# Kernel tuning notes

Measured on AMD Instinct MI355X. Metric: run time of the kernel, lower is better.

Reference implementation:

```python
import jax, jax.numpy as jnp
import numpy as np

B, N, D, G, K = 8, 4096, 64, 32, 16


def _knn_idx(pos, k, offset=1):
    # pos: (B, N, 3); exclude self via offset=1
    sq = jnp.sum(pos * pos, axis=-1)  # (B, N)
    dist = sq[:, :, None] + sq[:, None, :] - 2.0 * jnp.einsum('bnd,bmd->bnm', pos, pos)
    _, idx = jax.lax.top_k(-dist, k + offset)  # nearest first
    return idx[:, :, offset:]  # (B, N, k)


def _knn_group(x, idx):
    # x: (B, N, d), idx: (B, N, K) -> (B, N, K, d)
    return jax.vmap(lambda xb, ib: xb[ib])(x, idx)


def setup_inputs() -> dict:
    key = jax.random.key(0)
    ks = jax.random.split(key, 12)
    s = 0.02
    return {
        'x': jax.random.normal(ks[0], (B, N, D), jnp.float32),
        'pos': jax.random.normal(ks[1], (B, N, 3), jnp.float32),
        # layer_first: Linear(3d -> 4d) + relu, Linear(4d -> growth) + relu
        'W1': jax.random.normal(ks[2], (3 * D, 4 * D), jnp.float32) * s,
        'b1': jnp.zeros((4 * D,), jnp.float32),
        'W2': jax.random.normal(ks[3], (4 * D, G), jnp.float32) * s,
        'b2': jnp.zeros((G,), jnp.float32),
        # middle FCLayer: Linear(d+g -> g) + relu
        'Wmid': jax.random.normal(ks[4], (D + G, G), jnp.float32) * s,
        'bmid': jnp.zeros((G,), jnp.float32),
        # channel_gate2: Linear(d+2g -> d+2g)
        'Wg': jax.random.normal(ks[5], (D + 2 * G, D + 2 * G), jnp.float32) * s,
        'bg': jnp.zeros((D + 2 * G,), jnp.float32),
        # layer_last: Linear(d+2g -> g), no activation
        'Wlast': jax.random.normal(ks[6], (D + 2 * G, G), jnp.float32) * s,
        'blast': jnp.zeros((G,), jnp.float32),
    }


def reference(x, pos, W1, b1, W2, b2, Wmid, bmid, Wg, bg, Wlast, blast):
    knn_idx = _knn_idx(pos, K, offset=1)                 # (B, N, K)
    knn_feat = _knn_group(x, knn_idx)                    # (B, N, K, d)
    x_t = jnp.broadcast_to(x[:, :, None, :], knn_feat.shape)
    edge = jnp.concatenate([x_t, knn_feat, knn_feat - x_t], axis=-1)  # (B,N,K,3d)
    # layer_first: dense growth block
    h = jax.nn.relu(edge @ W1 + b1)
    h = jax.nn.relu(h @ W2 + b2)                          # (B,N,K,g)
    y = jnp.concatenate([h, x_t], axis=-1)               # (B,N,K,d+g)
    # middle layers (num_fc_layers-1 = 1 layer)
    y = jnp.concatenate([jax.nn.relu(y @ Wmid + bmid), y], axis=-1)  # (B,N,K,d+2g)
    # channel gate: mean over K, linear, sigmoid, scale
    gate = jax.nn.sigmoid(jnp.mean(y, axis=2) @ Wg + bg)  # (B,N,d+2g)
    y = y * gate[:, :, None, :]
    # layer_last (no activation) then concat
    y = jnp.concatenate([y @ Wlast + blast, y], axis=-1)   # (B,N,K,d+3g)
    # max aggregation over neighbors
    return jnp.max(y, axis=-2)                             # (B,N,d+3g)
```

## Files before the change

### kernel.cpp

```cpp
#include <hip/hip_runtime.h>
#include <stdint.h>

#define BB 8
#define NN 4096

typedef float f32x4 __attribute__((ext_vector_type(4)));
typedef short bf16x8 __attribute__((ext_vector_type(8)));
typedef bf16x8 bf16x8a __attribute__((may_alias));
#define MFMA16(a, b, c) __builtin_amdgcn_mfma_f32_16x16x32_bf16(a, b, c, 0, 0, 0)

static __device__ __forceinline__ short f2b(float f) {
    unsigned u = __float_as_uint(f);
    unsigned r = (u + 0x7FFFu + ((u >> 16) & 1u)) >> 16;
    return (short)r;
}
static __device__ __forceinline__ float b2f(short s) {
    return __uint_as_float(((unsigned)(unsigned short)s) << 16);
}
static __device__ __forceinline__ bf16x8 pack8(float4 a, float4 b) {
    bf16x8 v;
    v[0] = f2b(a.x); v[1] = f2b(a.y); v[2] = f2b(a.z); v[3] = f2b(a.w);
    v[4] = f2b(b.x); v[5] = f2b(b.y); v[6] = f2b(b.z); v[7] = f2b(b.w);
    return v;
}

__global__ __launch_bounds__(256)
void prep_kernel(const float* __restrict__ pos,
                 const float* __restrict__ W1, const float* __restrict__ W2,
                 const float* __restrict__ Wmid, const float* __restrict__ Wlast,
                 const float* __restrict__ Wg,
                 float4* __restrict__ pq,
                 short* __restrict__ W1T, short* __restrict__ W2T,
                 short* __restrict__ WmidT, short* __restrict__ WlastT,
                 short* __restrict__ WgT) {
    int t = blockIdx.x * 256 + threadIdx.x;
    if (t < 32768) {
        float x = pos[t * 3 + 0], y = pos[t * 3 + 1], z = pos[t * 3 + 2];
        float s = __fadd_rn(__fadd_rn(__fmul_rn(x, x), __fmul_rn(y, y)), __fmul_rn(z, z));
        pq[t] = make_float4(x, y, z, s);
    } else if (t < 81920) {
        int e = t - 32768; int col = e / 192, k = e - col * 192;
        W1T[e] = f2b(W1[(size_t)k * 256 + col]);
    } else if (t < 90112) {
        int e = t - 81920; int col = e >> 8, k = e & 255;
        W2T[e] = f2b(W2[(size_t)k * 32 + col]);
    } else if (t < 93184) {
        int e = t - 90112; int col = e / 96, k = e - col * 96;
        WmidT[e] = f2b(Wmid[(size_t)k * 32 + col]);
    } else if (t < 97280) {
        int e = t - 93184; int col = e >> 7, k = e & 127;
        WlastT[e] = f2b(Wlast[(size_t)k * 32 + col]);
    } else if (t < 113664) {
        int e = t - 97280; int col = e >> 7, k = e & 127;
        WgT[e] = f2b(Wg[(size_t)k * 128 + col]);
    }
}

static __device__ __forceinline__ float distf(float4 v, float qx, float qy,
                                              float qz, float qsq) {
    float dot = __fmaf_rn(v.z, qz, __fmaf_rn(v.y, qy, __fmul_rn(v.x, qx)));
    float d = __fsub_rn(__fadd_rn(qsq, v.w), __fmul_rn(2.0f, dot));
    return fmaxf(d, 0.0f);
}

__global__ __launch_bounds__(256)
void knn4_kernel(const float4* __restrict__ pq, int* __restrict__ out_idx) {
    __shared__ unsigned long long comp[4][160];

    const int w = threadIdx.x >> 6;
    const int l = threadIdx.x & 63;
    const int q = blockIdx.x * 4 + w;
    const int b = q >> 12, i = q & 4095;
    const int base = b << 12;
    const float INF = __uint_as_float(0x7F800000u);

    const float4 self = pq[base + i];
    const float qx = self.x, qy = self.y, qz = self.z, qsq = self.w;

    float lmin = INF;
#pragma unroll 4
    for (int t = 0; t < 64; ++t)
        lmin = fminf(lmin, distf(pq[base + t * 64 + l], qx, qy, qz, qsq));

    float cur = lmin, tau = INF;
    for (int r = 0; r < 17; ++r) {
        float m = cur;
#pragma unroll
        for (int o = 1; o < 64; o <<= 1) m = fminf(m, __shfl_xor(m, o));
        unsigned long long bal = __ballot(cur == m);
        if (l == (__ffsll((unsigned long long)bal) - 1)) cur = INF;
        tau = m;
    }

    int cbase = 0;
    const unsigned long long ltm = (l == 0) ? 0ull : ((~0ull) >> (64 - l));
    for (int t = 0; t < 64; ++t) {
        float d = distf(pq[base + t * 64 + l], qx, qy, qz, qsq);
        bool pr = (d <= tau);
        unsigned long long bb = __ballot(pr);
        if (pr) {
            int ps = cbase + __popcll(bb & ltm);
            if (ps < 160)
                comp[w][ps] = ((unsigned long long)__float_as_uint(d) << 32) |
                              (unsigned)(t * 64 + l);
        }
        cbase += __popcll(bb);
    }
    if (cbase > 160) cbase = 160;

    const unsigned long long INFK = ~0ull;
    unsigned long long ks[3];
#pragma unroll
    for (int s = 0; s < 3; ++s) {
        int e = s * 64 + l;
        ks[s] = (e < cbase) ? comp[w][e] : INFK;
    }
    unsigned keep = 0;
    for (int r = 0; r < 17; ++r) {
        unsigned long long ml = ks[0];
#pragma unroll
        for (int s = 1; s < 3; ++s) ml = (ks[s] < ml) ? ks[s] : ml;
        unsigned long long g = ml;
#pragma unroll
        for (int o = 1; o < 64; o <<= 1) {
            unsigned long long o2 = __shfl_xor(g, o);
            g = (o2 < g) ? o2 : g;
        }
        unsigned long long bb = __ballot(ml == g);
        if (l == (__ffsll(bb) - 1)) {
            bool done = false;
#pragma unroll
            for (int s = 0; s < 3; ++s)
                if (!done && ks[s] == g) { ks[s] = INFK; done = true; }
        }
        if (l == r - 1) keep = (unsigned)g;
    }
    if (l < 16) out_idx[(size_t)q * 16 + l] = (int)keep;
}

__global__ __launch_bounds__(256, 3)
void fused5_kernel(const float* __restrict__ x, const int* __restrict__ knn,
                   const short* __restrict__ W1T, const short* __restrict__ W2T,
                   const short* __restrict__ WmidT, const short* __restrict__ WlastT,
                   const short* __restrict__ WgT,
                   const float* __restrict__ b1, const float* __restrict__ b2,
                   const float* __restrict__ bmid, const float* __restrict__ bg,
                   const float* __restrict__ blast,
                   float* __restrict__ out) {
    __shared__ __align__(16) short s_h[64 * 264];
    __shared__ __align__(16) short s_y[64 * 136];
    __shared__ __align__(16) short s_ym[4 * 128];
    __shared__ float s_gate[4][128];

    const int w = threadIdx.x >> 6;
    const int l = threadIdx.x & 63;
    const int c16 = l & 15;
    const int qa = l >> 4;
    const int p = blockIdx.x * 4 + w;
    const int b = p >> 12;

    {
        const float* xrow = x + (size_t)p * 64;
        float4 xa = *(const float4*)(xrow + qa * 8);
        float4 xb = *(const float4*)(xrow + qa * 8 + 4);
        float4 xc = *(const float4*)(xrow + 32 + qa * 8);
        float4 xd = *(const float4*)(xrow + 32 + qa * 8 + 4);
        int nb = knn[(size_t)p * 16 + c16] & 4095;
        const float* nrow = x + ((size_t)(b << 12) + nb) * 64;
        float4 na = *(const float4*)(nrow + qa * 8);
        float4 nb4 = *(const float4*)(nrow + qa * 8 + 4);
        float4 nc = *(const float4*)(nrow + 32 + qa * 8);
        float4 nd = *(const float4*)(nrow + 32 + qa * 8 + 4);
        float4 da, db, dc, dd;
        da.x = na.x - xa.x; da.y = na.y - xa.y; da.z = na.z - xa.z; da.w = na.w - xa.w;
        db.x = nb4.x - xb.x; db.y = nb4.y - xb.y; db.z = nb4.z - xb.z; db.w = nb4.w - xb.w;
        dc.x = nc.x - xc.x; dc.y = nc.y - xc.y; dc.z = nc.z - xc.z; dc.w = nc.w - xc.w;
        dd.x = nd.x - xd.x; dd.y = nd.y - xd.y; dd.z = nd.z - xd.z; dd.w = nd.w - xd.w;
        bf16x8 pxa = pack8(xa, xb), pxc = pack8(xc, xd);
        int row = w * 16 + c16;
        short* sr = s_h + row * 264;
        *(bf16x8a*)(sr + qa * 8)       = pxa;
        *(bf16x8a*)(sr + 32 + qa * 8)  = pxc;
        *(bf16x8a*)(sr + 64 + qa * 8)  = pack8(na, nb4);
        *(bf16x8a*)(sr + 96 + qa * 8)  = pack8(nc, nd);
        *(bf16x8a*)(sr + 128 + qa * 8) = pack8(da, db);
        *(bf16x8a*)(sr + 160 + qa * 8) = pack8(dc, dd);
        short* yr = s_y + row * 136;
        *(bf16x8a*)(yr + 64 + qa * 8)  = pxa;
        *(bf16x8a*)(yr + 96 + qa * 8)  = pxc;
    }
    __syncthreads();

    f32x4 acc[4][4];
#pragma unroll
    for (int n = 0; n < 4; ++n) {
        float bv = b1[w * 64 + n * 16 + c16];
#pragma unroll
        for (int m = 0; m < 4; ++m) acc[m][n] = (f32x4){bv, bv, bv, bv};
    }
    {
        const short* w1p = W1T + (size_t)(w * 64 + c16) * 192 + qa * 8;
#pragma unroll
        for (int t = 0; t < 6; ++t) {
            bf16x8 av[4], bw[4];
#pragma unroll
            for (int m = 0; m < 4; ++m)
                av[m] = *(const bf16x8a*)(s_h + (m * 16 + c16) * 264 + t * 32 + qa * 8);
#pragma unroll
            for (int n = 0; n < 4; ++n)
                bw[n] = *(const bf16x8a*)(w1p + (size_t)n * 3072 + t * 32);
#pragma unroll
            for (int m = 0; m < 4; ++m)
#pragma unroll
                for (int n = 0; n < 4; ++n)
                    acc[m][n] = MFMA16(av[m], bw[n], acc[m][n]);
        }
    }
    __syncthreads();

#pragma unroll
    for (int m = 0; m < 4; ++m)
#pragma unroll
        for (int n = 0; n < 4; ++n)
#pragma unroll
            for (int r = 0; r < 4; ++r)
                s_h[(m * 16 + qa * 4 + r) * 264 + w * 64 + n * 16 + c16] =
                    f2b(fmaxf(acc[m][n][r], 0.f));
    __syncthreads();

    {
        f32x4 hacc[2];
        float h0 = b2[c16], h1v = b2[16 + c16];
        hacc[0] = (f32x4){h0, h0, h0, h0};
        hacc[1] = (f32x4){h1v, h1v, h1v, h1v};
#pragma unroll
        for (int t = 0; t < 8; ++t) {
            bf16x8 am = *(const bf16x8a*)(s_h + (w * 16 + c16) * 264 + t * 32 + qa * 8);
            bf16x8 wb0 = *(const bf16x8a*)(W2T + (size_t)c16 * 256 + t * 32 + qa * 8);
            bf16x8 wb1 = *(const bf16x8a*)(W2T + (size_t)(16 + c16) * 256 + t * 32 + qa * 8);
            hacc[0] = MFMA16(am, wb0, hacc[0]);
            hacc[1] = MFMA16(am, wb1, hacc[1]);
        }
#pragma unroll
        for (int n2 = 0; n2 < 2; ++n2)
#pragma unroll
            for (int r = 0; r < 4; ++r)
                s_y[(w * 16 + qa * 4 + r) * 136 + 32 + n2 * 16 + c16] =
                    f2b(fmaxf(hacc[n2][r], 0.f));
    }

    {
        f32x4 macc[2];
        float m0 = bmid[c16], m1 = bmid[16 + c16];
        macc[0] = (f32x4){m0, m0, m0, m0};
        macc[1] = (f32x4){m1, m1, m1, m1};
#pragma unroll
        for (int t = 0; t < 3; ++t) {
            bf16x8 av = *(const bf16x8a*)(s_y + (w * 16 + c16) * 136 + 32 + t * 32 + qa * 8);
            bf16x8 wb0 = *(const bf16x8a*)(WmidT + (size_t)c16 * 96 + t * 32 + qa * 8);
            bf16x8 wb1 = *(const bf16x8a*)(WmidT + (size_t)(16 + c16) * 96 + t * 32 + qa * 8);
            macc[0] = MFMA16(av, wb0, macc[0]);
            macc[1] = MFMA16(av, wb1, macc[1]);
        }
#pragma unroll
        for (int n2 = 0; n2 < 2; ++n2)
#pragma unroll
            for (int r = 0; r < 4; ++r)
                s_y[(w * 16 + qa * 4 + r) * 136 + n2 * 16 + c16] =
                    f2b(fmaxf(macc[n2][r], 0.f));
    }
    __syncthreads();

    {
        float s0 = 0.f, s1 = 0.f;
#pragma unroll
        for (int k = 0; k < 16; ++k) {
            const short* yp = s_y + (w * 16 + k) * 136;
            s0 += b2f(yp[2 * l]);
            s1 += b2f(yp[2 * l + 1]);
        }
        s_ym[w * 128 + 2 * l]     = f2b(s0 * 0.0625f);
        s_ym[w * 128 + 2 * l + 1] = f2b(s1 * 0.0625f);
    }
    __syncthreads();

    {
        f32x4 gacc[2];
        float g0 = bg[w * 32 + c16], g1 = bg[w * 32 + 16 + c16];
        gacc[0] = (f32x4){g0, g0, g0, g0};
        gacc[1] = (f32x4){g1, g1, g1, g1};
#pragma unroll
        for (int t = 0; t < 4; ++t) {
            bf16x8 av = *(const bf16x8a*)(s_ym + (c16 & 3) * 128 + t * 32 + qa * 8);
            bf16x8 wb0 = *(const bf16x8a*)(WgT + (size_t)(w * 32 + c16) * 128 + t * 32 + qa * 8);
            bf16x8 wb1 = *(const bf16x8a*)(WgT + (size_t)(w * 32 + 16 + c16) * 128 + t * 32 + qa * 8);
            gacc[0] = MFMA16(av, wb0, gacc[0]);
            gacc[1] = MFMA16(av, wb1, gacc[1]);
        }
        if (qa == 0) {
#pragma unroll
            for (int n2 = 0; n2 < 2; ++n2)
#pragma unroll
                for (int r = 0; r < 4; ++r)
                    s_gate[r][w * 32 + n2 * 16 + c16] =
                        1.0f / (1.0f + __expf(-gacc[n2][r]));
        }
    }
    __syncthreads();

    {
        float g0 = s_gate[w][2 * l], g1 = s_gate[w][2 * l + 1];
        float m0 = -__uint_as_float(0x7F800000u), m1 = m0;
#pragma unroll
        for (int k = 0; k < 16; ++k) {
            short* yp = s_y + (w * 16 + k) * 136;
            float v0 = b2f(yp[2 * l]) * g0;
            float v1 = b2f(yp[2 * l + 1]) * g1;
            m0 = fmaxf(m0, v0);
            m1 = fmaxf(m1, v1);
            yp[2 * l]     = f2b(v0);
            yp[2 * l + 1] = f2b(v1);
        }
        float2 st; st.x = m0; st.y = m1;
        *(float2*)(out + (size_t)p * 160 + 32 + 2 * l) = st;
    }
    __syncthreads();

    {
        f32x4 zacc[2];
        float z0 = blast[c16], z1 = blast[16 + c16];
        zacc[0] = (f32x4){z0, z0, z0, z0};
        zacc[1] = (f32x4){z1, z1, z1, z1};
#pragma unroll
        for (int t = 0; t < 4; ++t) {
            bf16x8 av = *(const bf16x8a*)(s_y + (w * 16 + c16) * 136 + t * 32 + qa * 8);
            bf16x8 wb0 = *(const bf16x8a*)(WlastT + (size_t)c16 * 128 + t * 32 + qa * 8);
            bf16x8 wb1 = *(const bf16x8a*)(WlastT + (size_t)(16 + c16) * 128 + t * 32 + qa * 8);
            zacc[0] = MFMA16(av, wb0, zacc[0]);
            zacc[1] = MFMA16(av, wb1, zacc[1]);
        }
#pragma unroll
        for (int nt = 0; nt < 2; ++nt) {
            float m = fmaxf(fmaxf(zacc[nt][0], zacc[nt][1]),
                            fmaxf(zacc[nt][2], zacc[nt][3]));
            m = fmaxf(m, __shfl_xor(m, 16));
            m = fmaxf(m, __shfl_xor(m, 32));
            if (l < 16) out[(size_t)p * 160 + nt * 16 + l] = m;
        }
    }
}

extern "C" void kernel_launch(void* const* d_in, const int* in_sizes, int n_in,
                              void* d_out, int out_size, void* d_ws, size_t ws_size,
                              hipStream_t stream) {
    const float* x     = (const float*)d_in[0];
    const float* pos   = (const float*)d_in[1];
    const float* W1    = (const float*)d_in[2];
    const float* b1    = (const float*)d_in[3];
    const float* W2    = (const float*)d_in[4];
    const float* b2    = (const float*)d_in[5];
    const float* Wmid  = (const float*)d_in[6];
    const float* bmid  = (const float*)d_in[7];
    const float* Wg    = (const float*)d_in[8];
    const float* bg    = (const float*)d_in[9];
    const float* Wlast = (const float*)d_in[10];
    const float* blast = (const float*)d_in[11];
    float* out = (float*)d_out;

    char* ws = (char*)d_ws;
    int*    idx    = (int*)(ws + 0);
    float4* pq     = (float4*)(ws + 2097152);
    short*  W1T    = (short*)(ws + 2621440);
    short*  W2T    = (short*)(ws + 2719744);
    short*  WmidT  = (short*)(ws + 2736128);
    short*  WlastT = (short*)(ws + 2742272);
    short*  WgT    = (short*)(ws + 2750464);

    prep_kernel<<<dim3(444), dim3(256), 0, stream>>>(
        pos, W1, W2, Wmid, Wlast, Wg, pq, W1T, W2T, WmidT, WlastT, WgT);
    knn4_kernel<<<dim3(BB * NN / 4), dim3(256), 0, stream>>>(pq, idx);
    fused5_kernel<<<dim3(BB * NN / 4), dim3(256), 0, stream>>>(
        x, idx, W1T, W2T, WmidT, WlastT, WgT, b1, b2, bmid, bg, blast, out);
}
```

Measured before the change: 507.4 us.

## Fuse KNN into MLP kernel, fold W1 edge weights, dedupe per-point x features

Moves the KNN search into the fused MLP kernel, so neighbor indices pass through a wave shuffle rather than a global buffer and a separate launch. Folds the [x, n, n-x] @ W1 concat algebraically into a 128-wide weight VT = [W1a-W1c; W1b+W1c], cutting the first GEMM's K dimension from 192 to 128. Also stores the per-point x (constant across the 16 neighbors) once per wave instead of per row, shrinking s_y and the gating/mean work. Risks higher register and LDS pressure in the combined kernel, plus small bf16 rounding differences from the pre-summed weights.

```diff
diff --git a/kernel.cpp b/kernel.cpp
--- a/kernel.cpp
+++ b/kernel.cpp
@@ -30,7 +30,7 @@
                  const float* __restrict__ Wmid, const float* __restrict__ Wlast,
                  const float* __restrict__ Wg,
                  float4* __restrict__ pq,
-                 short* __restrict__ W1T, short* __restrict__ W2T,
+                 short* __restrict__ VT, short* __restrict__ W2T,
                  short* __restrict__ WmidT, short* __restrict__ WlastT,
                  short* __restrict__ WgT) {
     int t = blockIdx.x * 256 + threadIdx.x;
@@ -38,20 +38,26 @@
         float x = pos[t * 3 + 0], y = pos[t * 3 + 1], z = pos[t * 3 + 2];
         float s = __fadd_rn(__fadd_rn(__fmul_rn(x, x), __fmul_rn(y, y)), __fmul_rn(z, z));
         pq[t] = make_float4(x, y, z, s);
-    } else if (t < 81920) {
-        int e = t - 32768; int col = e / 192, k = e - col * 192;
-        W1T[e] = f2b(W1[(size_t)k * 256 + col]);
-    } else if (t < 90112) {
-        int e = t - 81920; int col = e >> 8, k = e & 255;
+    } else if (t < 65536) {
+        int e = t - 32768; int col = e >> 7, k = e & 127;
+        float v;
+        if (k < 64) v = W1[(size_t)k * 256 + col] - W1[(size_t)(128 + k) * 256 + col];
+        else {
+            int j = k - 64;
+            v = W1[(size_t)(64 + j) * 256 + col] + W1[(size_t)(128 + j) * 256 + col];
+        }
+        VT[e] = f2b(v);
+    } else if (t < 73728) {
+        int e = t - 65536; int col = e >> 8, k = e & 255;
         W2T[e] = f2b(W2[(size_t)k * 32 + col]);
-    } else if (t < 93184) {
-        int e = t - 90112; int col = e / 96, k = e - col * 96;
+    } else if (t < 76800) {
+        int e = t - 73728; int col = e / 96, k = e - col * 96;
         WmidT[e] = f2b(Wmid[(size_t)k * 32 + col]);
+    } else if (t < 80896) {
+        int e = t - 76800; int col = e >> 7, k = e & 127;
+        WlastT[e] = f2b(Wlast[(size_t)k * 32 + col]);
     } else if (t < 97280) {
-        int e = t - 93184; int col = e >> 7, k = e & 127;
-        WlastT[e] = f2b(Wlast[(size_t)k * 32 + col]);
-    } else if (t < 113664) {
-        int e = t - 97280; int col = e >> 7, k = e & 127;
+        int e = t - 80896; int col = e >> 7, k = e & 127;
         WgT[e] = f2b(Wg[(size_t)k * 128 + col]);
     }
 }
@@ -63,84 +69,9 @@
     return fmaxf(d, 0.0f);
 }
 
-__global__ __launch_bounds__(256)
-void knn4_kernel(const float4* __restrict__ pq, int* __restrict__ out_idx) {
-    __shared__ unsigned long long comp[4][160];
-
-    const int w = threadIdx.x >> 6;
-    const int l = threadIdx.x & 63;
-    const int q = blockIdx.x * 4 + w;
-    const int b = q >> 12, i = q & 4095;
-    const int base = b << 12;
-    const float INF = __uint_as_float(0x7F800000u);
-
-    const float4 self = pq[base + i];
-    const float qx = self.x, qy = self.y, qz = self.z, qsq = self.w;
-
-    float lmin = INF;
-#pragma unroll 4
-    for (int t = 0; t < 64; ++t)
-        lmin = fminf(lmin, distf(pq[base + t * 64 + l], qx, qy, qz, qsq));
-
-    float cur = lmin, tau = INF;
-    for (int r = 0; r < 17; ++r) {
-        float m = cur;
-#pragma unroll
-        for (int o = 1; o < 64; o <<= 1) m = fminf(m, __shfl_xor(m, o));
-        unsigned long long bal = __ballot(cur == m);
-        if (l == (__ffsll((unsigned long long)bal) - 1)) cur = INF;
-        tau = m;
-    }
-
-    int cbase = 0;
-    const unsigned long long ltm = (l == 0) ? 0ull : ((~0ull) >> (64 - l));
-    for (int t = 0; t < 64; ++t) {
-        float d = distf(pq[base + t * 64 + l], qx, qy, qz, qsq);
-        bool pr = (d <= tau);
-        unsigned long long bb = __ballot(pr);
-        if (pr) {
-            int ps = cbase + __popcll(bb & ltm);
-            if (ps < 160)
-                comp[w][ps] = ((unsigned long long)__float_as_uint(d) << 32) |
-                              (unsigned)(t * 64 + l);
-        }
-        cbase += __popcll(bb);
-    }
-    if (cbase > 160) cbase = 160;
-
-    const unsigned long long INFK = ~0ull;
-    unsigned long long ks[3];
-#pragma unroll
-    for (int s = 0; s < 3; ++s) {
-        int e = s * 64 + l;
-        ks[s] = (e < cbase) ? comp[w][e] : INFK;
-    }
-    unsigned keep = 0;
-    for (int r = 0; r < 17; ++r) {
-        unsigned long long ml = ks[0];
-#pragma unroll
-        for (int s = 1; s < 3; ++s) ml = (ks[s] < ml) ? ks[s] : ml;
-        unsigned long long g = ml;
-#pragma unroll
-        for (int o = 1; o < 64; o <<= 1) {
-            unsigned long long o2 = __shfl_xor(g, o);
-            g = (o2 < g) ? o2 : g;
-        }
-        unsigned long long bb = __ballot(ml == g);
-        if (l == (__ffsll(bb) - 1)) {
-            bool done = false;
-#pragma unroll
-            for (int s = 0; s < 3; ++s)
-                if (!done && ks[s] == g) { ks[s] = INFK; done = true; }
-        }
-        if (l == r - 1) keep = (unsigned)g;
-    }
-    if (l < 16) out_idx[(size_t)q * 16 + l] = (int)keep;
-}
-
 __global__ __launch_bounds__(256, 3)
-void fused5_kernel(const float* __restrict__ x, const int* __restrict__ knn,
-                   const short* __restrict__ W1T, const short* __restrict__ W2T,
+void fused6_kernel(const float* __restrict__ x, const float4* __restrict__ pq,
+                   const short* __restrict__ VT, const short* __restrict__ W2T,
                    const short* __restrict__ WmidT, const short* __restrict__ WlastT,
                    const short* __restrict__ WgT,
                    const float* __restrict__ b1, const float* __restrict__ b2,
@@ -148,9 +79,12 @@
                    const float* __restrict__ blast,
                    float* __restrict__ out) {
     __shared__ __align__(16) short s_h[64 * 264];
-    __shared__ __align__(16) short s_y[64 * 136];
+    __shared__ __align__(16) short s_y[64 * 72];
+    __shared__ __align__(16) short s_x[4][64];
+    __shared__ __align__(16) short s_xg[4][64];
     __shared__ __align__(16) short s_ym[4 * 128];
     __shared__ float s_gate[4][128];
+    __shared__ unsigned long long comp[4][160];
 
     const int w = threadIdx.x >> 6;
     const int l = threadIdx.x & 63;
@@ -158,6 +92,73 @@
     const int qa = l >> 4;
     const int p = blockIdx.x * 4 + w;
     const int b = p >> 12;
+    const int base = b << 12;
+    const float INF = __uint_as_float(0x7F800000u);
+
+    unsigned keep = 0;
+    {
+        const float4 self = pq[base + (p & 4095)];
+        const float qx = self.x, qy = self.y, qz = self.z, qsq = self.w;
+
+        float lmin = INF;
+#pragma unroll 4
+        for (int t = 0; t < 64; ++t)
+            lmin = fminf(lmin, distf(pq[base + t * 64 + l], qx, qy, qz, qsq));
+
+        float cur = lmin, tau = INF;
+        for (int r = 0; r < 17; ++r) {
+            float m = cur;
+#pragma unroll
+            for (int o = 1; o < 64; o <<= 1) m = fminf(m, __shfl_xor(m, o));
+            unsigned long long bal = __ballot(cur == m);
+            if (l == (__ffsll(bal) - 1)) cur = INF;
+            tau = m;
+        }
+
+        int cbase = 0;
+        const unsigned long long ltm = (l == 0) ? 0ull : ((~0ull) >> (64 - l));
+        for (int t = 0; t < 64; ++t) {
+            float d = distf(pq[base + t * 64 + l], qx, qy, qz, qsq);
+            bool pr = (d <= tau);
+            unsigned long long bb = __ballot(pr);
+            if (pr) {
+                int ps = cbase + __popcll(bb & ltm);
+                if (ps < 160)
+                    comp[w][ps] = ((unsigned long long)__float_as_uint(d) << 32) |
+                                  (unsigned)(t * 64 + l);
+            }
+            cbase += __popcll(bb);
+        }
+        if (cbase > 160) cbase = 160;
+
+        const unsigned long long INFK = ~0ull;
+        unsigned long long ks[3];
+#pragma unroll
+        for (int s = 0; s < 3; ++s) {
+            int e = s * 64 + l;
+            ks[s] = (e < cbase) ? comp[w][e] : INFK;
+        }
+        for (int r = 0; r < 17; ++r) {
+            unsigned long long ml = ks[0];
+#pragma unroll
+            for (int s = 1; s < 3; ++s) ml = (ks[s] < ml) ? ks[s] : ml;
+            unsigned long long g = ml;
+#pragma unroll
+            for (int o = 1; o < 64; o <<= 1) {
+                unsigned long long o2 = __shfl_xor(g, o);
+                g = (o2 < g) ? o2 : g;
+            }
+            unsigned long long bb = __ballot(ml == g);
+            if (l == (__ffsll(bb) - 1)) {
+                bool done = false;
+#pragma unroll
+                for (int s = 0; s < 3; ++s)
+                    if (!done && ks[s] == g) { ks[s] = INFK; done = true; }
+            }
+            if (l == r - 1) keep = (unsigned)g;
+        }
+    }
+    const int nb = __shfl((int)keep, c16) & 4095;
 
     {
         const float* xrow = x + (size_t)p * 64;
@@ -165,29 +166,22 @@
         float4 xb = *(const float4*)(xrow + qa * 8 + 4);
         float4 xc = *(const float4*)(xrow + 32 + qa * 8);
         float4 xd = *(const float4*)(xrow + 32 + qa * 8 + 4);
-        int nb = knn[(size_t)p * 16 + c16] & 4095;
-        const float* nrow = x + ((size_t)(b << 12) + nb) * 64;
+        const float* nrow = x + ((size_t)base + nb) * 64;
         float4 na = *(const float4*)(nrow + qa * 8);
         float4 nb4 = *(const float4*)(nrow + qa * 8 + 4);
         float4 nc = *(const float4*)(nrow + 32 + qa * 8);
         float4 nd = *(const float4*)(nrow + 32 + qa * 8 + 4);
-        float4 da, db, dc, dd;
-        da.x = na.x - xa.x; da.y = na.y - xa.y; da.z = na.z - xa.z; da.w = na.w - xa.w;
-        db.x = nb4.x - xb.x; db.y = nb4.y - xb.y; db.z = nb4.z - xb.z; db.w = nb4.w - xb.w;
-        dc.x = nc.x - xc.x; dc.y = nc.y - xc.y; dc.z = nc.z - xc.z; dc.w = nc.w - xc.w;
-        dd.x = nd.x - xd.x; dd.y = nd.y - xd.y; dd.z = nd.z - xd.z; dd.w = nd.w - xd.w;
         bf16x8 pxa = pack8(xa, xb), pxc = pack8(xc, xd);
         int row = w * 16 + c16;
         short* sr = s_h + row * 264;
-        *(bf16x8a*)(sr + qa * 8)       = pxa;
-        *(bf16x8a*)(sr + 32 + qa * 8)  = pxc;
-        *(bf16x8a*)(sr + 64 + qa * 8)  = pack8(na, nb4);
-        *(bf16x8a*)(sr + 96 + qa * 8)  = pack8(nc, nd);
-        *(bf16x8a*)(sr + 128 + qa * 8) = pack8(da, db);
-        *(bf16x8a*)(sr + 160 + qa * 8) = pack8(dc, dd);
-        short* yr = s_y + row * 136;
-        *(bf16x8a*)(yr + 64 + qa * 8)  = pxa;
-        *(bf16x8a*)(yr + 96 + qa * 8)  = pxc;
+        *(bf16x8a*)(sr + qa * 8)      = pxa;
+        *(bf16x8a*)(sr + 32 + qa * 8) = pxc;
+        *(bf16x8a*)(sr + 64 + qa * 8) = pack8(na, nb4);
+        *(bf16x8a*)(sr + 96 + qa * 8) = pack8(nc, nd);
+        if (c16 == 0) {
+            *(bf16x8a*)(&s_x[w][qa * 8])      = pxa;
+            *(bf16x8a*)(&s_x[w][32 + qa * 8]) = pxc;
+        }
     }
     __syncthreads();
 
@@ -199,16 +193,16 @@
         for (int m = 0; m < 4; ++m) acc[m][n] = (f32x4){bv, bv, bv, bv};
     }
     {
-        const short* w1p = W1T + (size_t)(w * 64 + c16) * 192 + qa * 8;
-#pragma unroll
-        for (int t = 0; t < 6; ++t) {
+        const short* w1p = VT + (size_t)(w * 64 + c16) * 128 + qa * 8;
+#pragma unroll
+        for (int t = 0; t < 4; ++t) {
             bf16x8 av[4], bw[4];
 #pragma unroll
             for (int m = 0; m < 4; ++m)
                 av[m] = *(const bf16x8a*)(s_h + (m * 16 + c16) * 264 + t * 32 + qa * 8);
 #pragma unroll
             for (int n = 0; n < 4; ++n)
-                bw[n] = *(const bf16x8a*)(w1p + (size_t)n * 3072 + t * 32);
+                bw[n] = *(const bf16x8a*)(w1p + (size_t)n * 2048 + t * 32);
 #pragma unroll
             for (int m = 0; m < 4; ++m)
 #pragma unroll
@@ -245,7 +239,7 @@
         for (int n2 = 0; n2 < 2; ++n2)
 #pragma unroll
             for (int r = 0; r < 4; ++r)
-                s_y[(w * 16 + qa * 4 + r) * 136 + 32 + n2 * 16 + c16] =
+                s_y[(w * 16 + qa * 4 + r) * 72 + 32 + n2 * 16 + c16] =
                     f2b(fmaxf(hacc[n2][r], 0.f));
     }
 
@@ -256,7 +250,10 @@
         macc[1] = (f32x4){m1, m1, m1, m1};
 #pragma unroll
         for (int t = 0; t < 3; ++t) {
-            bf16x8 av = *(const bf16x8a*)(s_y + (w * 16 + c16) * 136 + 32 + t * 32 + qa * 8);
+            bf16x8 av;
+            if (t == 0)      av = *(const bf16x8a*)(s_y + (w * 16 + c16) * 72 + 32 + qa * 8);
+            else if (t == 1) av = *(const bf16x8a*)(&s_x[w][qa * 8]);
+            else             av = *(const bf16x8a*)(&s_x[w][32 + qa * 8]);
             bf16x8 wb0 = *(const bf16x8a*)(WmidT + (size_t)c16 * 96 + t * 32 + qa * 8);
             bf16x8 wb1 = *(const bf16x8a*)(WmidT + (size_t)(16 + c16) * 96 + t * 32 + qa * 8);
             macc[0] = MFMA16(av, wb0, macc[0]);
@@ -266,21 +263,17 @@
         for (int n2 = 0; n2 < 2; ++n2)
 #pragma unroll
             for (int r = 0; r < 4; ++r)
-                s_y[(w * 16 + qa * 4 + r) * 136 + n2 * 16 + c16] =
+                s_y[(w * 16 + qa * 4 + r) * 72 + n2 * 16 + c16] =
                     f2b(fmaxf(macc[n2][r], 0.f));
     }
     __syncthreads();
 
     {
-        float s0 = 0.f, s1 = 0.f;
-#pragma unroll
-        for (int k = 0; k < 16; ++k) {
-            const short* yp = s_y + (w * 16 + k) * 136;
-            s0 += b2f(yp[2 * l]);
-            s1 += b2f(yp[2 * l + 1]);
-        }
-        s_ym[w * 128 + 2 * l]     = f2b(s0 * 0.0625f);
-        s_ym[w * 128 + 2 * l + 1] = f2b(s1 * 0.0625f);
+        float s0 = 0.f;
+#pragma unroll
+        for (int k = 0; k < 16; ++k) s0 += b2f(s_y[(w * 16 + k) * 72 + l]);
+        s_ym[w * 128 + l]      = f2b(s0 * 0.0625f);
+        s_ym[w * 128 + 64 + l] = s_x[w][l];
     }
     __syncthreads();
 
@@ -309,20 +302,20 @@
     __syncthreads();
 
     {
-        float g0 = s_gate[w][2 * l], g1 = s_gate[w][2 * l + 1];
-        float m0 = -__uint_as_float(0x7F800000u), m1 = m0;
+        float gy = s_gate[w][l];
+        float m0 = -INF;
 #pragma unroll
         for (int k = 0; k < 16; ++k) {
-            short* yp = s_y + (w * 16 + k) * 136;
-            float v0 = b2f(yp[2 * l]) * g0;
-            float v1 = b2f(yp[2 * l + 1]) * g1;
-            m0 = fmaxf(m0, v0);
-            m1 = fmaxf(m1, v1);
-            yp[2 * l]     = f2b(v0);
-            yp[2 * l + 1] = f2b(v1);
-        }
-        float2 st; st.x = m0; st.y = m1;
-        *(float2*)(out + (size_t)p * 160 + 32 + 2 * l) = st;
+            short* yp = s_y + (w * 16 + k) * 72 + l;
+            float v = b2f(*yp) * gy;
+            m0 = fmaxf(m0, v);
+            *yp = f2b(v);
+        }
+        out[(size_t)p * 160 + 32 + l] = m0;
+        float gx = s_gate[w][64 + l];
+        float xv = b2f(s_x[w][l]) * gx;
+        out[(size_t)p * 160 + 96 + l] = xv;
+        s_xg[w][l] = f2b(xv);
     }
     __syncthreads();
 
@@ -333,7 +326,11 @@
         zacc[1] = (f32x4){z1, z1, z1, z1};
 #pragma unroll
         for (int t = 0; t < 4; ++t) {
-            bf16x8 av = *(const bf16x8a*)(s_y + (w * 16 + c16) * 136 + t * 32 + qa * 8);
+            bf16x8 av;
+            if (t == 0)      av = *(const bf16x8a*)(s_y + (w * 16 + c16) * 72 + qa * 8);
+            else if (t == 1) av = *(const bf16x8a*)(s_y + (w * 16 + c16) * 72 + 32 + qa * 8);
+            else if (t == 2) av = *(const bf16x8a*)(&s_xg[w][qa * 8]);
+            else             av = *(const bf16x8a*)(&s_xg[w][32 + qa * 8]);
             bf16x8 wb0 = *(const bf16x8a*)(WlastT + (size_t)c16 * 128 + t * 32 + qa * 8);
             bf16x8 wb1 = *(const bf16x8a*)(WlastT + (size_t)(16 + c16) * 128 + t * 32 + qa * 8);
             zacc[0] = MFMA16(av, wb0, zacc[0]);
@@ -368,17 +365,15 @@
     float* out = (float*)d_out;
 
     char* ws = (char*)d_ws;
-    int*    idx    = (int*)(ws + 0);
-    float4* pq     = (float4*)(ws + 2097152);
-    short*  W1T    = (short*)(ws + 2621440);
-    short*  W2T    = (short*)(ws + 2719744);
-    short*  WmidT  = (short*)(ws + 2736128);
-    short*  WlastT = (short*)(ws + 2742272);
-    short*  WgT    = (short*)(ws + 2750464);
-
-    prep_kernel<<<dim3(444), dim3(256), 0, stream>>>(
-        pos, W1, W2, Wmid, Wlast, Wg, pq, W1T, W2T, WmidT, WlastT, WgT);
-    knn4_kernel<<<dim3(BB * NN / 4), dim3(256), 0, stream>>>(pq, idx);
-    fused5_kernel<<<dim3(BB * NN / 4), dim3(256), 0, stream>>>(
-        x, idx, W1T, W2T, WmidT, WlastT, WgT, b1, b2, bmid, bg, blast, out);
-}
+    float4* pq     = (float4*)(ws + 0);
+    short*  VT     = (short*)(ws + 524288);
+    short*  W2T    = (short*)(ws + 589824);
+    short*  WmidT  = (short*)(ws + 606208);
+    short*  WlastT = (short*)(ws + 612352);
+    short*  WgT    = (short*)(ws + 620544);
+
+    prep_kernel<<<dim3(380), dim3(256), 0, stream>>>(
+        pos, W1, W2, Wmid, Wlast, Wg, pq, VT, W2T, WmidT, WlastT, WgT);
+    fused6_kernel<<<dim3(BB * NN / 4), dim3(256), 0, stream>>>(
+        x, pq, VT, W2T, WmidT, WlastT, WgT, b1, b2, bmid, bg, blast, out);
+}
```

Measured after the change: 566.3 us. 11.6% more time.
